# Performance work log

Hardware: AMD Instinct MI355X
Metric: run time of the kernel (lower is better)

Reference implementation:

```python
import jax, jax.numpy as jnp
import numpy as np

NEG_SLOPE = 0.2
EPS = 1e-16

def gat_conv(x, edge_index, W, a_src, a_dst, b):
    # x: [N, Fin], W: [Fin, C], a_src/a_dst: [C], b: [C]
    N = x.shape[0]
    src, dst = edge_index[0], edge_index[1]
    h = x @ W                                  # [N, C]
    alpha_s = h @ a_src                        # [N]
    alpha_d = h @ a_dst                        # [N]
    e = alpha_s[src] + alpha_d[dst]            # [E]
    e = jnp.where(e > 0, e, NEG_SLOPE * e)     # LeakyReLU(0.2)
    # ragged softmax over incoming edges of each dst node
    m = jax.ops.segment_max(e, dst, num_segments=N)       # [N]
    p = jnp.exp(e - m[dst])                                # [E]
    s = jax.ops.segment_sum(p, dst, num_segments=N)        # [N]
    alpha = p / (s[dst] + EPS)                             # [E]
    out = jax.ops.segment_sum(alpha[:, None] * h[src], dst, num_segments=N)
    return out + b

def setup_inputs() -> dict:
    key = jax.random.key(0)
    ks = jax.random.split(key, 10)
    N, Fin, H, C, E = 50000, 128, 64, 64, 800000
    x = jax.random.normal(ks[0], (N, Fin), dtype=jnp.float32)
    edge_index = jax.random.randint(ks[1], (2, E), 0, N, dtype=jnp.int64)
    sc1 = 1.0 / np.sqrt(Fin)
    sc2 = 1.0 / np.sqrt(H)
    W1 = jax.random.normal(ks[2], (Fin, H), dtype=jnp.float32) * sc1
    a_src1 = jax.random.normal(ks[3], (H,), dtype=jnp.float32) * sc2
    a_dst1 = jax.random.normal(ks[4], (H,), dtype=jnp.float32) * sc2
    b1 = jnp.zeros((H,), dtype=jnp.float32)
    W2 = jax.random.normal(ks[5], (H, C), dtype=jnp.float32) * sc2
    a_src2 = jax.random.normal(ks[6], (C,), dtype=jnp.float32) * sc2
    a_dst2 = jax.random.normal(ks[7], (C,), dtype=jnp.float32) * sc2
    b2 = jnp.zeros((C,), dtype=jnp.float32)
    return {"x": x, "edge_index": edge_index, "W1": W1, "a_src1": a_src1,
            "a_dst1": a_dst1, "b1": b1, "W2": W2, "a_src2": a_src2,
            "a_dst2": a_dst2, "b2": b2}

def reference(x, edge_index, W1, a_src1, a_dst1, b1, W2, a_src2, a_dst2, b2):
    h = gat_conv(x, edge_index, W1, a_src1, a_dst1, b1)
    h = jax.nn.relu(h)
    out = gat_conv(h, edge_index, W2, a_src2, a_dst2, b2)
    return out
```

## Files before the change

kernel.cpp:

```cpp
#include <hip/hip_runtime.h>
#include <cstddef>

constexpr int FIN = 128;
constexpr int EPB = 4096;
constexpr int BSH = 7;
constexpr int NPB = 128;

typedef _Float16 half4 __attribute__((ext_vector_type(4)));
typedef _Float16 half8 __attribute__((ext_vector_type(8)));
typedef float floatx4 __attribute__((ext_vector_type(4)));

__device__ __forceinline__ int block_excl_scan_256(int v, int tid, int* wsums) {
    int lane = tid & 63, w = tid >> 6;
    int x = v;
#pragma unroll
    for (int off = 1; off < 64; off <<= 1) {
        int y = __shfl_up(x, off, 64);
        if (lane >= off) x += y;
    }
    if (lane == 63) wsums[w] = x;
    __syncthreads();
    int add = 0;
#pragma unroll
    for (int i = 0; i < 4; ++i) add += (i < w) ? wsums[i] : 0;
    return x + add - v;
}

template <int K, typename XT>
__device__ __forceinline__
void gemm_mfma_body(const XT* __restrict__ X, const float* __restrict__ W,
                    const float* __restrict__ ASRC, const float* __restrict__ ADST,
                    _Float16* __restrict__ Hh, float* __restrict__ AS,
                    float* __restrict__ AD, int N, int blk,
                    _Float16* Xh, _Float16* WT) {
    constexpr int LDH = K + 8;
    const int tid = threadIdx.x;
    const int nb = blk * 64;

    if constexpr (sizeof(XT) == 4) {
        constexpr int QPR = K / 4;
        for (int i = tid; i < 64 * QPR; i += 256) {
            int r = i / QPR, q = i % QPR;
            float4 v = make_float4(0.f, 0.f, 0.f, 0.f);
            if (nb + r < N) v = *(const float4*)(X + (size_t)(nb + r) * K + 4 * q);
            half4 h; h[0] = (_Float16)v.x; h[1] = (_Float16)v.y;
            h[2] = (_Float16)v.z; h[3] = (_Float16)v.w;
            *(half4*)(Xh + r * LDH + 4 * q) = h;
        }
    } else {
        constexpr int OPR = K / 8;
        for (int i = tid; i < 64 * OPR; i += 256) {
            int r = i / OPR, o = i % OPR;
            half8 v = {};
            if (nb + r < N) v = *(const half8*)(X + (size_t)(nb + r) * K + 8 * o);
            *(half8*)(Xh + r * LDH + 8 * o) = v;
        }
    }
    for (int i = tid; i < 64 * (K / 4); i += 256) {
        int n = i & 63, kg = i >> 6;
        half4 h;
#pragma unroll
        for (int j = 0; j < 4; ++j)
            h[j] = (_Float16)W[(4 * kg + j) * 64 + n];
        *(half4*)(WT + n * LDH + 4 * kg) = h;
    }
    __syncthreads();

    const int l = tid & 63;
    const int r0 = (tid >> 6) * 16;
    const int n16 = l & 15, quad = l >> 4;

    floatx4 acc[4];
#pragma unroll
    for (int nt = 0; nt < 4; ++nt) acc[nt] = (floatx4){0.f, 0.f, 0.f, 0.f};

#pragma unroll
    for (int k0 = 0; k0 < K; k0 += 32) {
        half8 a = *(const half8*)(Xh + (r0 + n16) * LDH + k0 + quad * 8);
#pragma unroll
        for (int nt = 0; nt < 4; ++nt) {
            half8 b = *(const half8*)(WT + (nt * 16 + n16) * LDH + k0 + quad * 8);
            acc[nt] = __builtin_amdgcn_mfma_f32_16x16x32_f16(a, b, acc[nt], 0, 0, 0);
        }
    }

    float pa[4] = {0.f, 0.f, 0.f, 0.f}, pd[4] = {0.f, 0.f, 0.f, 0.f};
#pragma unroll
    for (int nt = 0; nt < 4; ++nt) {
        float as_v = ASRC[nt * 16 + n16], ad_v = ADST[nt * 16 + n16];
#pragma unroll
        for (int reg = 0; reg < 4; ++reg) {
            pa[reg] += acc[nt][reg] * as_v;
            pd[reg] += acc[nt][reg] * ad_v;
        }
    }
#pragma unroll
    for (int off = 1; off < 16; off <<= 1) {
#pragma unroll
        for (int reg = 0; reg < 4; ++reg) {
            pa[reg] += __shfl_xor(pa[reg], off, 64);
            pd[reg] += __shfl_xor(pd[reg], off, 64);
        }
    }
    if (n16 == 0) {
#pragma unroll
        for (int reg = 0; reg < 4; ++reg) {
            int row = nb + r0 + quad * 4 + reg;
            if (row < N) { AS[row] = pa[reg]; AD[row] = pd[reg]; }
        }
    }

#pragma unroll
    for (int nt = 0; nt < 4; ++nt)
#pragma unroll
        for (int reg = 0; reg < 4; ++reg)
            Xh[(r0 + quad * 4 + reg) * LDH + nt * 16 + n16] = (_Float16)acc[nt][reg];
    {
        int r = r0 + (l >> 2);
        int o = (l & 3) * 16;
        if (nb + r < N) {
            half8 v0 = *(const half8*)(Xh + r * LDH + o);
            half8 v1 = *(const half8*)(Xh + r * LDH + o + 8);
            *(half8*)(Hh + (size_t)(nb + r) * 64 + o) = v0;
            *(half8*)(Hh + (size_t)(nb + r) * 64 + o + 8) = v1;
        }
    }
}

__global__ __launch_bounds__(256)
void gemm1_and_count(const float* __restrict__ X, const float* __restrict__ W,
                     const float* __restrict__ ASRC, const float* __restrict__ ADST,
                     _Float16* __restrict__ Hh, float* __restrict__ AS,
                     float* __restrict__ AD, int N,
                     const int* __restrict__ dst, int E, int nblk, int nbuckp,
                     int* __restrict__ cnts, int* __restrict__ ticket) {
    constexpr int K = FIN, LDH = K + 8;
    __shared__ _Float16 Xh[64 * LDH];
    __shared__ _Float16 WT[64 * LDH];

    const int tid = threadIdx.x;
    if ((int)blockIdx.x < nblk) {
        int* hist = (int*)Xh;
        if (blockIdx.x == 0 && tid == 0) *ticket = 0;
        for (int i = tid; i < nbuckp; i += 256) hist[i] = 0;
        __syncthreads();
        int e0 = blockIdx.x * EPB;
        int e1 = min(e0 + EPB, E);
        for (int e = e0 + tid; e < e1; e += 256)
            atomicAdd(&hist[dst[e] >> BSH], 1);
        __syncthreads();
        for (int i = tid; i < nbuckp; i += 256)
            cnts[blockIdx.x * nbuckp + i] = hist[i];
        return;
    }
    gemm_mfma_body<K, float>(X, W, ASRC, ADST, Hh, AS, AD, N,
                             blockIdx.x - nblk, Xh, WT);
}

template <int K, typename XT>
__global__ __launch_bounds__(256)
void gemm_feat(const XT* __restrict__ X, const float* __restrict__ W,
               const float* __restrict__ ASRC, const float* __restrict__ ADST,
               _Float16* __restrict__ Hh, float* __restrict__ AS,
               float* __restrict__ AD, int N) {
    constexpr int LDH = K + 8;
    __shared__ _Float16 Xh[64 * LDH];
    __shared__ _Float16 WT[64 * LDH];
    gemm_mfma_body<K, XT>(X, W, ASRC, ADST, Hh, AS, AD, N, blockIdx.x, Xh, WT);
}

__global__ __launch_bounds__(256)
void bucket_colscan_fused(int* __restrict__ cnts, int nblk, int nbuckp,
                          int nbuck, int E, int* __restrict__ btotal,
                          int* __restrict__ bbase, int* __restrict__ ticket) {
    __shared__ int wsums[4];
    __shared__ int ws2[4];
    __shared__ int lastflag;
    int b = blockIdx.x;
    int tid = threadIdx.x;
    int v = (tid < nblk) ? cnts[tid * nbuckp + b] : 0;
    int excl = block_excl_scan_256(v, tid, wsums);
    if (tid < nblk) cnts[tid * nbuckp + b] = excl;
    if (tid == nblk) {
        atomicExch(&btotal[b], excl);
        int old = atomicAdd(ticket, 1);
        lastflag = (old == nbuck - 1);
    }
    __syncthreads();
    if (!lastflag) return;
    int i0 = 2 * tid, i1 = 2 * tid + 1;
    int v0 = (i0 < nbuck) ? atomicAdd(&btotal[i0], 0) : 0;
    int v1 = (i1 < nbuck) ? atomicAdd(&btotal[i1], 0) : 0;
    __syncthreads();
    int e2 = block_excl_scan_256(v0 + v1, tid, ws2);
    if (i0 <= nbuck) bbase[i0] = e2;
    if (i1 <= nbuck) bbase[i1] = e2 + v0;
}

__global__ __launch_bounds__(256)
void bucket_scatter(const int* __restrict__ src, const int* __restrict__ dst,
                    int E, int nbuckp, const int* __restrict__ cnts,
                    const int* __restrict__ bbase, int* __restrict__ ebuck) {
    __shared__ int cur[512];
    int tid = threadIdx.x;
    for (int i = tid; i < nbuckp; i += 256)
        cur[i] = bbase[i] + cnts[blockIdx.x * nbuckp + i];
    __syncthreads();
    int e0 = blockIdx.x * EPB;
    int e1 = min(e0 + EPB, E);
    for (int e = e0 + tid; e < e1; e += 256) {
        int d = dst[e];
        int p = atomicAdd(&cur[d >> BSH], 1);
        ebuck[p] = ((d & (NPB - 1)) << 25) | src[e];
    }
}

__global__ __launch_bounds__(256)
void bucket_to_csr(const int* __restrict__ ebuck, const int* __restrict__ bbase,
                   int N, int E, int* __restrict__ row_ptr,
                   int* __restrict__ csr_src) {
    __shared__ int hist[NPB];
    __shared__ int cur[NPB];
    __shared__ int wsums[4];
    int b = blockIdx.x, tid = threadIdx.x;
    int nstart = b << BSH;
    int base = bbase[b], endp = bbase[b + 1];
    if (tid < NPB) hist[tid] = 0;
    __syncthreads();
    for (int e = base + tid; e < endp; e += 256)
        atomicAdd(&hist[((unsigned)ebuck[e]) >> 25], 1);
    __syncthreads();
    int v = (tid < NPB) ? hist[tid] : 0;
    int excl = block_excl_scan_256(v, tid, wsums);
    if (tid < NPB) {
        cur[tid] = excl;
        if (nstart + tid < N) row_ptr[nstart + tid] = base + excl;
    }
    if (b == 0 && tid == 0) row_ptr[N] = E;
    __syncthreads();
    for (int e = base + tid; e < endp; e += 256) {
        int pv = ebuck[e];
        int p = atomicAdd(&cur[((unsigned)pv) >> 25], 1);
        csr_src[base + p] = pv & 0x1FFFFFF;
    }
}

template <typename OT>
__global__ __launch_bounds__(256)
void gat_aggregate(const _Float16* __restrict__ Hh, const float* __restrict__ AS,
                   const float* __restrict__ AD, const int* __restrict__ row_ptr,
                   const int* __restrict__ csr_src, const float* __restrict__ bias,
                   OT* __restrict__ OUT, int N, int relu) {
    const int lane = threadIdx.x & 63;
    const int n = blockIdx.x * 4 + (threadIdx.x >> 6);
    if (n >= N) return;

    const int base = row_ptr[n], end = row_ptr[n + 1];
    const int cnt = end - base;
    const float adn = AD[n];

    if (cnt > 64) {
        float m = -INFINITY;
        for (int c0 = base; c0 < end; c0 += 64) {
            int c = min(64, end - c0);
            float e = -INFINITY;
            if (lane < c) {
                int sr = csr_src[c0 + lane];
                float t = AS[sr] + adn;
                e = t > 0.f ? t : 0.2f * t;
            }
#pragma unroll
            for (int off = 32; off > 0; off >>= 1) e = fmaxf(e, __shfl_xor(e, off, 64));
            m = fmaxf(m, e);
        }
        float s = 0.f, acc = 0.f;
        for (int c0 = base; c0 < end; c0 += 64) {
            int c = min(64, end - c0);
            int srcl = 0;
            float p = 0.f;
            if (lane < c) {
                srcl = csr_src[c0 + lane];
                float t = AS[srcl] + adn;
                t = t > 0.f ? t : 0.2f * t;
                p = __expf(t - m);
            }
            float cs = p;
#pragma unroll
            for (int off = 32; off > 0; off >>= 1) cs += __shfl_xor(cs, off, 64);
            s += cs;
            for (int j = 0; j < c; ++j)
                acc += __shfl(p, j, 64) *
                       (float)Hh[(size_t)__shfl(srcl, j, 64) * 64 + lane];
        }
        float o = acc * (1.f / (s + 1e-16f)) + bias[lane];
        if (relu) o = fmaxf(o, 0.f);
        OUT[(size_t)n * 64 + lane] = (OT)o;
        return;
    }

    int srcl = 0;
    float el = -INFINITY;
    if (lane < cnt) {
        srcl = csr_src[base + lane];
        float e = AS[srcl] + adn;
        el = e > 0.f ? e : 0.2f * e;
    }
    float m = el;
#pragma unroll
    for (int off = 32; off > 0; off >>= 1) m = fmaxf(m, __shfl_xor(m, off, 64));
    float p = (lane < cnt) ? __expf(el - m) : 0.f;
    float s = p;
#pragma unroll
    for (int off = 32; off > 0; off >>= 1) s += __shfl_xor(s, off, 64);
    const float inv = 1.f / (s + 1e-16f);

    const int eg = lane >> 3;
    const int c8 = (lane & 7) * 8;

    float acc[8], acc2[8];
#pragma unroll
    for (int t = 0; t < 8; ++t) { acc[t] = 0.f; acc2[t] = 0.f; }

    int j = 0;
    for (; j + 16 <= cnt; j += 16) {
        int iA = j + eg, iB = j + 8 + eg;
        int sA = __shfl(srcl, iA, 64), sB = __shfl(srcl, iB, 64);
        float aA = __shfl(p, iA, 64),  aB = __shfl(p, iB, 64);
        half8 hA = *(const half8*)(Hh + (size_t)sA * 64 + c8);
        half8 hB = *(const half8*)(Hh + (size_t)sB * 64 + c8);
#pragma unroll
        for (int t = 0; t < 8; ++t) {
            acc[t]  += aA * (float)hA[t];
            acc2[t] += aB * (float)hB[t];
        }
    }
    for (; j < cnt; j += 8) {
        int iA = j + eg;
        int sA = __shfl(srcl, iA, 64);
        float aA = __shfl(p, iA, 64);
        half8 hA = *(const half8*)(Hh + (size_t)sA * 64 + c8);
#pragma unroll
        for (int t = 0; t < 8; ++t) acc[t] += aA * (float)hA[t];
    }
#pragma unroll
    for (int t = 0; t < 8; ++t) acc[t] += acc2[t];
#pragma unroll
    for (int off = 8; off <= 32; off <<= 1)
#pragma unroll
        for (int t = 0; t < 8; ++t) acc[t] += __shfl_xor(acc[t], off, 64);

    if (lane < 8) {
        float4 b0 = *(const float4*)(bias + c8);
        float4 b1 = *(const float4*)(bias + c8 + 4);
        float o[8];
        o[0] = acc[0] * inv + b0.x; o[1] = acc[1] * inv + b0.y;
        o[2] = acc[2] * inv + b0.z; o[3] = acc[3] * inv + b0.w;
        o[4] = acc[4] * inv + b1.x; o[5] = acc[5] * inv + b1.y;
        o[6] = acc[6] * inv + b1.z; o[7] = acc[7] * inv + b1.w;
        if (relu) {
#pragma unroll
            for (int t = 0; t < 8; ++t) o[t] = fmaxf(o[t], 0.f);
        }
        if constexpr (sizeof(OT) == 2) {
            half8 hv;
#pragma unroll
            for (int t = 0; t < 8; ++t) hv[t] = (_Float16)o[t];
            *(half8*)((_Float16*)OUT + (size_t)n * 64 + c8) = hv;
        } else {
            *(float4*)((float*)OUT + (size_t)n * 64 + c8) =
                make_float4(o[0], o[1], o[2], o[3]);
            *(float4*)((float*)OUT + (size_t)n * 64 + c8 + 4) =
                make_float4(o[4], o[5], o[6], o[7]);
        }
    }
}

extern "C" void kernel_launch(void* const* d_in, const int* in_sizes, int n_in,
                              void* d_out, int out_size, void* d_ws, size_t ws_size,
                              hipStream_t stream) {
    const float* x    = (const float*)d_in[0];
    const int*   ei   = (const int*)d_in[1];
    const float* W1   = (const float*)d_in[2];
    const float* as1w = (const float*)d_in[3];
    const float* ad1w = (const float*)d_in[4];
    const float* b1   = (const float*)d_in[5];
    const float* W2   = (const float*)d_in[6];
    const float* as2w = (const float*)d_in[7];
    const float* ad2w = (const float*)d_in[8];
    const float* b2   = (const float*)d_in[9];
    float* out = (float*)d_out;

    const int N = in_sizes[0] / FIN;
    const int E = in_sizes[1] / 2;
    const int* esrc = ei;
    const int* edst = ei + E;

    const int nbuck = (N + NPB - 1) >> BSH;
    const int nbuckp = nbuck;
    const int nblk = (E + EPB - 1) / EPB;

    char* wp8 = (char*)d_ws;
    _Float16* Hh  = (_Float16*)wp8;  wp8 += (size_t)N * 64 * 2;
    _Float16* R1h = (_Float16*)wp8;  wp8 += (size_t)N * 64 * 2;
    float* AS1 = (float*)wp8;        wp8 += (size_t)N * 4;
    float* AD1 = (float*)wp8;        wp8 += (size_t)N * 4;
    float* AS2 = (float*)wp8;        wp8 += (size_t)N * 4;
    float* AD2 = (float*)wp8;        wp8 += (size_t)N * 4;
    int* row_ptr = (int*)wp8;        wp8 += (size_t)(N + 1) * 4;
    int* csr     = (int*)wp8;        wp8 += (size_t)E * 4;
    int* ebuck   = (int*)wp8;        wp8 += (size_t)E * 4;
    int* cnts    = (int*)wp8;        wp8 += (size_t)nblk * nbuckp * 4;
    int* btotal  = (int*)wp8;        wp8 += (size_t)nbuck * 4;
    int* bbase   = (int*)wp8;        wp8 += (size_t)(nbuck + 1) * 4;
    int* ticket  = (int*)wp8;        wp8 += 4;

    const int nbG = (N + 63) / 64;

    hipLaunchKernelGGL(gemm1_and_count, dim3(nblk + nbG), dim3(256), 0, stream,
                       x, W1, as1w, ad1w, Hh, AS1, AD1, N,
                       edst, E, nblk, nbuckp, cnts, ticket);
    hipLaunchKernelGGL(bucket_colscan_fused, dim3(nbuck), dim3(256), 0, stream,
                       cnts, nblk, nbuckp, nbuck, E, btotal, bbase, ticket);
    hipLaunchKernelGGL(bucket_scatter, dim3(nblk), dim3(256), 0, stream,
                       esrc, edst, E, nbuckp, cnts, bbase, ebuck);
    hipLaunchKernelGGL(bucket_to_csr, dim3(nbuck), dim3(256), 0, stream,
                       ebuck, bbase, N, E, row_ptr, csr);
    hipLaunchKernelGGL(gat_aggregate<_Float16>, dim3((N + 3) / 4), dim3(256), 0,
                       stream, Hh, AS1, AD1, row_ptr, csr, b1, R1h, N, 1);
    hipLaunchKernelGGL((gemm_feat<64, _Float16>), dim3(nbG), dim3(256), 0, stream,
                       R1h, W2, as2w, ad2w, Hh, AS2, AD2, N);
    hipLaunchKernelGGL(gat_aggregate<float>, dim3((N + 3) / 4), dim3(256), 0,
                       stream, Hh, AS2, AD2, row_ptr, csr, b2, out, N, 0);
}
```

Before: 191.6 us.

## Split feature matrices into two 32-column halves and aggregate in two passes

Stores H and the layer-1 result as two separate 32-channel fp16 arrays. Each GAT aggregation becomes two kernels: the first computes the softmax, stores normalised alphas per edge and aggregates the first half, and the second reuses those alphas for the other half. The aim is to shrink each gather's working set so it stays cache-resident. The cost is an extra launch per layer, a per-edge alpha buffer that is written and re-read, and a second read of the CSR arrays. It also halves EPB and makes the column scan loop so that more than 256 count blocks are supported.

```diff
diff --git a/kernel.cpp b/kernel.cpp
--- a/kernel.cpp
+++ b/kernel.cpp
@@ -1,16 +1,18 @@
 #include <hip/hip_runtime.h>
 #include <cstddef>
 
-constexpr int FIN = 128;
-constexpr int EPB = 4096;
-constexpr int BSH = 7;
-constexpr int NPB = 128;
+constexpr int FIN  = 128;
+constexpr int EPB  = 2048;
+constexpr int BSH  = 7;
+constexpr int NPB  = 128;
+constexpr int PACK_SH = 25;
 
 typedef _Float16 half4 __attribute__((ext_vector_type(4)));
 typedef _Float16 half8 __attribute__((ext_vector_type(8)));
 typedef float floatx4 __attribute__((ext_vector_type(4)));
 
-__device__ __forceinline__ int block_excl_scan_256(int v, int tid, int* wsums) {
+__device__ __forceinline__ int block_scan_tot(int v, int tid, int* wsums,
+                                              int* tot) {
     int lane = tid & 63, w = tid >> 6;
     int x = v;
 #pragma unroll
@@ -23,37 +25,43 @@
     int add = 0;
 #pragma unroll
     for (int i = 0; i < 4; ++i) add += (i < w) ? wsums[i] : 0;
+    *tot = wsums[0] + wsums[1] + wsums[2] + wsums[3];
     return x + add - v;
 }
 
-template <int K, typename XT>
+template <int K, bool SPLIT>
 __device__ __forceinline__
-void gemm_mfma_body(const XT* __restrict__ X, const float* __restrict__ W,
+void gemm_mfma_body(const float* __restrict__ Xf,
+                    const _Float16* __restrict__ XA,
+                    const _Float16* __restrict__ XB,
+                    const float* __restrict__ W,
                     const float* __restrict__ ASRC, const float* __restrict__ ADST,
-                    _Float16* __restrict__ Hh, float* __restrict__ AS,
-                    float* __restrict__ AD, int N, int blk,
-                    _Float16* Xh, _Float16* WT) {
+                    _Float16* __restrict__ HA, _Float16* __restrict__ HB,
+                    float* __restrict__ AS, float* __restrict__ AD,
+                    int N, int blk, _Float16* Xh, _Float16* WT) {
     constexpr int LDH = K + 8;
     const int tid = threadIdx.x;
     const int nb = blk * 64;
 
-    if constexpr (sizeof(XT) == 4) {
+    if constexpr (!SPLIT) {
         constexpr int QPR = K / 4;
         for (int i = tid; i < 64 * QPR; i += 256) {
             int r = i / QPR, q = i % QPR;
             float4 v = make_float4(0.f, 0.f, 0.f, 0.f);
-            if (nb + r < N) v = *(const float4*)(X + (size_t)(nb + r) * K + 4 * q);
+            if (nb + r < N) v = *(const float4*)(Xf + (size_t)(nb + r) * K + 4 * q);
             half4 h; h[0] = (_Float16)v.x; h[1] = (_Float16)v.y;
             h[2] = (_Float16)v.z; h[3] = (_Float16)v.w;
             *(half4*)(Xh + r * LDH + 4 * q) = h;
         }
     } else {
-        constexpr int OPR = K / 8;
-        for (int i = tid; i < 64 * OPR; i += 256) {
-            int r = i / OPR, o = i % OPR;
-            half8 v = {};
-            if (nb + r < N) v = *(const half8*)(X + (size_t)(nb + r) * K + 8 * o);
-            *(half8*)(Xh + r * LDH + 8 * o) = v;
+        for (int i = tid; i < 64 * 16; i += 256) {
+            int r = i >> 4, ch = i & 15;
+            half4 v = {};
+            if (nb + r < N) {
+                if (ch < 8) v = *(const half4*)(XA + (size_t)(nb + r) * 32 + 4 * ch);
+                else        v = *(const half4*)(XB + (size_t)(nb + r) * 32 + 4 * (ch - 8));
+            }
+            *(half4*)(Xh + r * LDH + 4 * ch) = v;
         }
     }
     for (int i = tid; i < 64 * (K / 4); i += 256) {
@@ -121,8 +129,13 @@
         if (nb + r < N) {
             half8 v0 = *(const half8*)(Xh + r * LDH + o);
             half8 v1 = *(const half8*)(Xh + r * LDH + o + 8);
-            *(half8*)(Hh + (size_t)(nb + r) * 64 + o) = v0;
-            *(half8*)(Hh + (size_t)(nb + r) * 64 + o + 8) = v1;
+            if (o < 32) {
+                *(half8*)(HA + (size_t)(nb + r) * 32 + o) = v0;
+                *(half8*)(HA + (size_t)(nb + r) * 32 + o + 8) = v1;
+            } else {
+                *(half8*)(HB + (size_t)(nb + r) * 32 + (o - 32)) = v0;
+                *(half8*)(HB + (size_t)(nb + r) * 32 + (o - 32) + 8) = v1;
+            }
         }
     }
 }
@@ -130,9 +143,9 @@
 __global__ __launch_bounds__(256)
 void gemm1_and_count(const float* __restrict__ X, const float* __restrict__ W,
                      const float* __restrict__ ASRC, const float* __restrict__ ADST,
-                     _Float16* __restrict__ Hh, float* __restrict__ AS,
-                     float* __restrict__ AD, int N,
-                     const int* __restrict__ dst, int E, int nblk, int nbuckp,
+                     _Float16* __restrict__ HA, _Float16* __restrict__ HB,
+                     float* __restrict__ AS, float* __restrict__ AD, int N,
+                     const int* __restrict__ dst, int E, int nblk, int nbuck,
                      int* __restrict__ cnts, int* __restrict__ ticket) {
     constexpr int K = FIN, LDH = K + 8;
     __shared__ _Float16 Xh[64 * LDH];
@@ -142,47 +155,54 @@
     if ((int)blockIdx.x < nblk) {
         int* hist = (int*)Xh;
         if (blockIdx.x == 0 && tid == 0) *ticket = 0;
-        for (int i = tid; i < nbuckp; i += 256) hist[i] = 0;
+        for (int i = tid; i < nbuck; i += 256) hist[i] = 0;
         __syncthreads();
         int e0 = blockIdx.x * EPB;
         int e1 = min(e0 + EPB, E);
         for (int e = e0 + tid; e < e1; e += 256)
             atomicAdd(&hist[dst[e] >> BSH], 1);
         __syncthreads();
-        for (int i = tid; i < nbuckp; i += 256)
-            cnts[blockIdx.x * nbuckp + i] = hist[i];
+        for (int i = tid; i < nbuck; i += 256)
+            cnts[blockIdx.x * nbuck + i] = hist[i];
         return;
     }
-    gemm_mfma_body<K, float>(X, W, ASRC, ADST, Hh, AS, AD, N,
-                             blockIdx.x - nblk, Xh, WT);
-}
-
-template <int K, typename XT>
-__global__ __launch_bounds__(256)
-void gemm_feat(const XT* __restrict__ X, const float* __restrict__ W,
-               const float* __restrict__ ASRC, const float* __restrict__ ADST,
-               _Float16* __restrict__ Hh, float* __restrict__ AS,
-               float* __restrict__ AD, int N) {
-    constexpr int LDH = K + 8;
+    gemm_mfma_body<K, false>(X, nullptr, nullptr, W, ASRC, ADST, HA, HB,
+                             AS, AD, N, blockIdx.x - nblk, Xh, WT);
+}
+
+__global__ __launch_bounds__(256)
+void gemm2_feat(const _Float16* __restrict__ XA, const _Float16* __restrict__ XB,
+                const float* __restrict__ W,
+                const float* __restrict__ ASRC, const float* __restrict__ ADST,
+                _Float16* __restrict__ HA, _Float16* __restrict__ HB,
+                float* __restrict__ AS, float* __restrict__ AD, int N) {
+    constexpr int LDH = 64 + 8;
     __shared__ _Float16 Xh[64 * LDH];
     __shared__ _Float16 WT[64 * LDH];
-    gemm_mfma_body<K, XT>(X, W, ASRC, ADST, Hh, AS, AD, N, blockIdx.x, Xh, WT);
-}
-
-__global__ __launch_bounds__(256)
-void bucket_colscan_fused(int* __restrict__ cnts, int nblk, int nbuckp,
-                          int nbuck, int E, int* __restrict__ btotal,
-                          int* __restrict__ bbase, int* __restrict__ ticket) {
+    gemm_mfma_body<64, true>(nullptr, XA, XB, W, ASRC, ADST, HA, HB,
+                             AS, AD, N, blockIdx.x, Xh, WT);
+}
+
+__global__ __launch_bounds__(256)
+void bucket_colscan_fused(int* __restrict__ cnts, int nblk, int nbuck,
+                          int* __restrict__ btotal, int* __restrict__ bbase,
+                          int* __restrict__ ticket) {
     __shared__ int wsums[4];
-    __shared__ int ws2[4];
     __shared__ int lastflag;
     int b = blockIdx.x;
     int tid = threadIdx.x;
-    int v = (tid < nblk) ? cnts[tid * nbuckp + b] : 0;
-    int excl = block_excl_scan_256(v, tid, wsums);
-    if (tid < nblk) cnts[tid * nbuckp + b] = excl;
-    if (tid == nblk) {
-        atomicExch(&btotal[b], excl);
+    int carry = 0;
+    for (int c0 = 0; c0 < nblk; c0 += 256) {
+        int t = c0 + tid;
+        int v = (t < nblk) ? cnts[t * nbuck + b] : 0;
+        int tot;
+        int e = block_scan_tot(v, tid, wsums, &tot);
+        if (t < nblk) cnts[t * nbuck + b] = e + carry;
+        carry += tot;
+        __syncthreads();
+    }
+    if (tid == 0) {
+        atomicExch(&btotal[b], carry);
         int old = atomicAdd(ticket, 1);
         lastflag = (old == nbuck - 1);
     }
@@ -192,26 +212,27 @@
     int v0 = (i0 < nbuck) ? atomicAdd(&btotal[i0], 0) : 0;
     int v1 = (i1 < nbuck) ? atomicAdd(&btotal[i1], 0) : 0;
     __syncthreads();
-    int e2 = block_excl_scan_256(v0 + v1, tid, ws2);
+    int tot2;
+    int e2 = block_scan_tot(v0 + v1, tid, wsums, &tot2);
     if (i0 <= nbuck) bbase[i0] = e2;
     if (i1 <= nbuck) bbase[i1] = e2 + v0;
 }
 
 __global__ __launch_bounds__(256)
 void bucket_scatter(const int* __restrict__ src, const int* __restrict__ dst,
-                    int E, int nbuckp, const int* __restrict__ cnts,
+                    int E, int nbuck, const int* __restrict__ cnts,
                     const int* __restrict__ bbase, int* __restrict__ ebuck) {
     __shared__ int cur[512];
     int tid = threadIdx.x;
-    for (int i = tid; i < nbuckp; i += 256)
-        cur[i] = bbase[i] + cnts[blockIdx.x * nbuckp + i];
+    for (int i = tid; i < nbuck; i += 256)
+        cur[i] = bbase[i] + cnts[blockIdx.x * nbuck + i];
     __syncthreads();
     int e0 = blockIdx.x * EPB;
     int e1 = min(e0 + EPB, E);
     for (int e = e0 + tid; e < e1; e += 256) {
         int d = dst[e];
         int p = atomicAdd(&cur[d >> BSH], 1);
-        ebuck[p] = ((d & (NPB - 1)) << 25) | src[e];
+        ebuck[p] = ((d & (NPB - 1)) << PACK_SH) | src[e];
     }
 }
 
@@ -228,10 +249,11 @@
     if (tid < NPB) hist[tid] = 0;
     __syncthreads();
     for (int e = base + tid; e < endp; e += 256)
-        atomicAdd(&hist[((unsigned)ebuck[e]) >> 25], 1);
+        atomicAdd(&hist[((unsigned)ebuck[e]) >> PACK_SH], 1);
     __syncthreads();
     int v = (tid < NPB) ? hist[tid] : 0;
-    int excl = block_excl_scan_256(v, tid, wsums);
+    int tot;
+    int excl = block_scan_tot(v, tid, wsums, &tot);
     if (tid < NPB) {
         cur[tid] = excl;
         if (nstart + tid < N) row_ptr[nstart + tid] = base + excl;
@@ -240,21 +262,21 @@
     __syncthreads();
     for (int e = base + tid; e < endp; e += 256) {
         int pv = ebuck[e];
-        int p = atomicAdd(&cur[((unsigned)pv) >> 25], 1);
-        csr_src[base + p] = pv & 0x1FFFFFF;
+        int p = atomicAdd(&cur[((unsigned)pv) >> PACK_SH], 1);
+        csr_src[base + p] = pv & ((1 << PACK_SH) - 1);
     }
 }
 
 template <typename OT>
 __global__ __launch_bounds__(256)
-void gat_aggregate(const _Float16* __restrict__ Hh, const float* __restrict__ AS,
-                   const float* __restrict__ AD, const int* __restrict__ row_ptr,
-                   const int* __restrict__ csr_src, const float* __restrict__ bias,
-                   OT* __restrict__ OUT, int N, int relu) {
+void gat_aggA(const _Float16* __restrict__ HA, const float* __restrict__ AS,
+              const float* __restrict__ AD, const int* __restrict__ row_ptr,
+              const int* __restrict__ csr_src, float* __restrict__ alphaB,
+              const float* __restrict__ bias, OT* __restrict__ OUT,
+              int N, int relu) {
     const int lane = threadIdx.x & 63;
     const int n = blockIdx.x * 4 + (threadIdx.x >> 6);
     if (n >= N) return;
-
     const int base = row_ptr[n], end = row_ptr[n + 1];
     const int cnt = end - base;
     const float adn = AD[n];
@@ -273,28 +295,46 @@
             for (int off = 32; off > 0; off >>= 1) e = fmaxf(e, __shfl_xor(e, off, 64));
             m = fmaxf(m, e);
         }
-        float s = 0.f, acc = 0.f;
+        float s = 0.f;
         for (int c0 = base; c0 < end; c0 += 64) {
             int c = min(64, end - c0);
-            int srcl = 0;
             float p = 0.f;
             if (lane < c) {
-                srcl = csr_src[c0 + lane];
-                float t = AS[srcl] + adn;
+                int sr = csr_src[c0 + lane];
+                float t = AS[sr] + adn;
                 t = t > 0.f ? t : 0.2f * t;
                 p = __expf(t - m);
+                alphaB[c0 + lane] = p;
             }
             float cs = p;
 #pragma unroll
             for (int off = 32; off > 0; off >>= 1) cs += __shfl_xor(cs, off, 64);
             s += cs;
-            for (int j = 0; j < c; ++j)
-                acc += __shfl(p, j, 64) *
-                       (float)Hh[(size_t)__shfl(srcl, j, 64) * 64 + lane];
-        }
-        float o = acc * (1.f / (s + 1e-16f)) + bias[lane];
-        if (relu) o = fmaxf(o, 0.f);
-        OUT[(size_t)n * 64 + lane] = (OT)o;
+        }
+        float inv = 1.f / (s + 1e-16f);
+        float acc = 0.f;
+        for (int c0 = base; c0 < end; c0 += 64) {
+            int c = min(64, end - c0);
+            int sr = 0; float p = 0.f;
+            if (lane < c) {
+                sr = csr_src[c0 + lane];
+                p = alphaB[c0 + lane] * inv;
+                alphaB[c0 + lane] = p;
+            }
+            for (int j = 0; j < c; ++j) {
+                float a = __shfl(p, j, 64);
+                int sj = __shfl(sr, j, 64);
+                if (lane < 32) acc += a * (float)HA[(size_t)sj * 32 + lane];
+            }
+        }
+        if (lane < 32) {
+            float o = acc + bias[lane];
+            if (relu) o = fmaxf(o, 0.f);
+            if constexpr (sizeof(OT) == 2)
+                ((_Float16*)OUT)[(size_t)n * 32 + lane] = (_Float16)o;
+            else
+                ((float*)OUT)[(size_t)n * 64 + lane] = o;
+        }
         return;
     }
 
@@ -313,23 +353,22 @@
 #pragma unroll
     for (int off = 32; off > 0; off >>= 1) s += __shfl_xor(s, off, 64);
     const float inv = 1.f / (s + 1e-16f);
+    const float al = p * inv;
+    if (lane < cnt) alphaB[base + lane] = al;
 
     const int eg = lane >> 3;
-    const int c8 = (lane & 7) * 8;
-
-    float acc[8], acc2[8];
-#pragma unroll
-    for (int t = 0; t < 8; ++t) { acc[t] = 0.f; acc2[t] = 0.f; }
-
+    const int c4 = (lane & 7) * 4;
+
+    float acc[4] = {0.f, 0.f, 0.f, 0.f}, acc2[4] = {0.f, 0.f, 0.f, 0.f};
     int j = 0;
     for (; j + 16 <= cnt; j += 16) {
         int iA = j + eg, iB = j + 8 + eg;
         int sA = __shfl(srcl, iA, 64), sB = __shfl(srcl, iB, 64);
-        float aA = __shfl(p, iA, 64),  aB = __shfl(p, iB, 64);
-        half8 hA = *(const half8*)(Hh + (size_t)sA * 64 + c8);
-        half8 hB = *(const half8*)(Hh + (size_t)sB * 64 + c8);
-#pragma unroll
-        for (int t = 0; t < 8; ++t) {
+        float aA = __shfl(al, iA, 64), aB = __shfl(al, iB, 64);
+        half4 hA = *(const half4*)(HA + (size_t)sA * 32 + c4);
+        half4 hB = *(const half4*)(HA + (size_t)sB * 32 + c4);
+#pragma unroll
+        for (int t = 0; t < 4; ++t) {
             acc[t]  += aA * (float)hA[t];
             acc2[t] += aB * (float)hB[t];
         }
@@ -337,40 +376,126 @@
     for (; j < cnt; j += 8) {
         int iA = j + eg;
         int sA = __shfl(srcl, iA, 64);
-        float aA = __shfl(p, iA, 64);
-        half8 hA = *(const half8*)(Hh + (size_t)sA * 64 + c8);
-#pragma unroll
-        for (int t = 0; t < 8; ++t) acc[t] += aA * (float)hA[t];
-    }
-#pragma unroll
-    for (int t = 0; t < 8; ++t) acc[t] += acc2[t];
+        float aA = __shfl(al, iA, 64);
+        half4 hA = *(const half4*)(HA + (size_t)sA * 32 + c4);
+#pragma unroll
+        for (int t = 0; t < 4; ++t) acc[t] += aA * (float)hA[t];
+    }
+#pragma unroll
+    for (int t = 0; t < 4; ++t) acc[t] += acc2[t];
 #pragma unroll
     for (int off = 8; off <= 32; off <<= 1)
 #pragma unroll
-        for (int t = 0; t < 8; ++t) acc[t] += __shfl_xor(acc[t], off, 64);
+        for (int t = 0; t < 4; ++t) acc[t] += __shfl_xor(acc[t], off, 64);
 
     if (lane < 8) {
-        float4 b0 = *(const float4*)(bias + c8);
-        float4 b1 = *(const float4*)(bias + c8 + 4);
-        float o[8];
-        o[0] = acc[0] * inv + b0.x; o[1] = acc[1] * inv + b0.y;
-        o[2] = acc[2] * inv + b0.z; o[3] = acc[3] * inv + b0.w;
-        o[4] = acc[4] * inv + b1.x; o[5] = acc[5] * inv + b1.y;
-        o[6] = acc[6] * inv + b1.z; o[7] = acc[7] * inv + b1.w;
+        float4 bv = *(const float4*)(bias + c4);
+        float o[4] = {acc[0] + bv.x, acc[1] + bv.y, acc[2] + bv.z, acc[3] + bv.w};
         if (relu) {
 #pragma unroll
-            for (int t = 0; t < 8; ++t) o[t] = fmaxf(o[t], 0.f);
+            for (int t = 0; t < 4; ++t) o[t] = fmaxf(o[t], 0.f);
         }
         if constexpr (sizeof(OT) == 2) {
-            half8 hv;
-#pragma unroll
-            for (int t = 0; t < 8; ++t) hv[t] = (_Float16)o[t];
-            *(half8*)((_Float16*)OUT + (size_t)n * 64 + c8) = hv;
+            half4 hv; hv[0] = (_Float16)o[0]; hv[1] = (_Float16)o[1];
+            hv[2] = (_Float16)o[2]; hv[3] = (_Float16)o[3];
+            *(half4*)((_Float16*)OUT + (size_t)n * 32 + c4) = hv;
         } else {
-            *(float4*)((float*)OUT + (size_t)n * 64 + c8) =
+            *(float4*)((float*)OUT + (size_t)n * 64 + c4) =
                 make_float4(o[0], o[1], o[2], o[3]);
-            *(float4*)((float*)OUT + (size_t)n * 64 + c8 + 4) =
-                make_float4(o[4], o[5], o[6], o[7]);
+        }
+    }
+}
+
+template <typename OT>
+__global__ __launch_bounds__(256)
+void gat_aggB(const _Float16* __restrict__ HB, const int* __restrict__ row_ptr,
+              const int* __restrict__ csr_src, const float* __restrict__ alphaB,
+              const float* __restrict__ bias, OT* __restrict__ OUT,
+              int N, int relu) {
+    const int lane = threadIdx.x & 63;
+    const int n = blockIdx.x * 4 + (threadIdx.x >> 6);
+    if (n >= N) return;
+    const int base = row_ptr[n], end = row_ptr[n + 1];
+    const int cnt = end - base;
+
+    if (cnt > 64) {
+        float acc = 0.f;
+        for (int c0 = base; c0 < end; c0 += 64) {
+            int c = min(64, end - c0);
+            int sr = 0; float a = 0.f;
+            if (lane < c) {
+                sr = csr_src[c0 + lane];
+                a = alphaB[c0 + lane];
+            }
+            for (int j = 0; j < c; ++j) {
+                float aj = __shfl(a, j, 64);
+                int sj = __shfl(sr, j, 64);
+                if (lane < 32) acc += aj * (float)HB[(size_t)sj * 32 + lane];
+            }
+        }
+        if (lane < 32) {
+            float o = acc + bias[32 + lane];
+            if (relu) o = fmaxf(o, 0.f);
+            if constexpr (sizeof(OT) == 2)
+                ((_Float16*)OUT)[(size_t)n * 32 + lane] = (_Float16)o;
+            else
+                ((float*)OUT)[(size_t)n * 64 + 32 + lane] = o;
+        }
+        return;
+    }
+
+    int srcl = 0;
+    float al = 0.f;
+    if (lane < cnt) {
+        srcl = csr_src[base + lane];
+        al = alphaB[base + lane];
+    }
+    const int eg = lane >> 3;
+    const int c4 = (lane & 7) * 4;
+
+    float acc[4] = {0.f, 0.f, 0.f, 0.f}, acc2[4] = {0.f, 0.f, 0.f, 0.f};
+    int j = 0;
+    for (; j + 16 <= cnt; j += 16) {
+        int iA = j + eg, iB = j + 8 + eg;
+        int sA = __shfl(srcl, iA, 64), sB = __shfl(srcl, iB, 64);
+        float aA = __shfl(al, iA, 64), aB = __shfl(al, iB, 64);
+        half4 hA = *(const half4*)(HB + (size_t)sA * 32 + c4);
+        half4 hB = *(const half4*)(HB + (size_t)sB * 32 + c4);
+#pragma unroll
+        for (int t = 0; t < 4; ++t) {
+            acc[t]  += aA * (float)hA[t];
+            acc2[t] += aB * (float)hB[t];
+        }
+    }
+    for (; j < cnt; j += 8) {
+        int iA = j + eg;
+        int sA = __shfl(srcl, iA, 64);
+        float aA = __shfl(al, iA, 64);
+        half4 hA = *(const half4*)(HB + (size_t)sA * 32 + c4);
+#pragma unroll
+        for (int t = 0; t < 4; ++t) acc[t] += aA * (float)hA[t];
+    }
+#pragma unroll
+    for (int t = 0; t < 4; ++t) acc[t] += acc2[t];
+#pragma unroll
+    for (int off = 8; off <= 32; off <<= 1)
+#pragma unroll
+        for (int t = 0; t < 4; ++t) acc[t] += __shfl_xor(acc[t], off, 64);
+
+    if (lane < 8) {
+        float4 bv = *(const float4*)(bias + 32 + c4);
+        float o[4] = {acc[0] + bv.x, acc[1] + bv.y, acc[2] + bv.z, acc[3] + bv.w};
+        if (relu) {
+#pragma unroll
+            for (int t = 0; t < 4; ++t) o[t] = fmaxf(o[t], 0.f);
+        }
+        if constexpr (sizeof(OT) == 2) {
+            half4 hv; hv[0] = (_Float16)o[0]; hv[1] = (_Float16)o[1];
+            hv[2] = (_Float16)o[2]; hv[3] = (_Float16)o[3];
+            *(half4*)((_Float16*)OUT + (size_t)n * 32 + c4) = hv;
+        } else {
+            *(float4*)((float*)OUT + (size_t)n * 64 + 32 + c4) =
+                make_float4(o[0], o[1], o[2], o[3]);
         }
     }
 }
@@ -396,39 +521,46 @@
     const int* edst = ei + E;
 
     const int nbuck = (N + NPB - 1) >> BSH;
-    const int nbuckp = nbuck;
-    const int nblk = (E + EPB - 1) / EPB;
+    const int nblk  = (E + EPB - 1) / EPB;
 
     char* wp8 = (char*)d_ws;
-    _Float16* Hh  = (_Float16*)wp8;  wp8 += (size_t)N * 64 * 2;
-    _Float16* R1h = (_Float16*)wp8;  wp8 += (size_t)N * 64 * 2;
+    _Float16* HhA = (_Float16*)wp8;  wp8 += (size_t)N * 32 * 2;
+    _Float16* HhB = (_Float16*)wp8;  wp8 += (size_t)N * 32 * 2;
+    _Float16* R1A = (_Float16*)wp8;  wp8 += (size_t)N * 32 * 2;
+    _Float16* R1B = (_Float16*)wp8;  wp8 += (size_t)N * 32 * 2;
     float* AS1 = (float*)wp8;        wp8 += (size_t)N * 4;
     float* AD1 = (float*)wp8;        wp8 += (size_t)N * 4;
     float* AS2 = (float*)wp8;        wp8 += (size_t)N * 4;
     float* AD2 = (float*)wp8;        wp8 += (size_t)N * 4;
+    float* alphaB = (float*)wp8;     wp8 += (size_t)E * 4;
     int* row_ptr = (int*)wp8;        wp8 += (size_t)(N + 1) * 4;
     int* csr     = (int*)wp8;        wp8 += (size_t)E * 4;
     int* ebuck   = (int*)wp8;        wp8 += (size_t)E * 4;
-    int* cnts    = (int*)wp8;        wp8 += (size_t)nblk * nbuckp * 4;
+    int* cnts    = (int*)wp8;        wp8 += (size_t)nblk * nbuck * 4;
     int* btotal  = (int*)wp8;        wp8 += (size_t)nbuck * 4;
     int* bbase   = (int*)wp8;        wp8 += (size_t)(nbuck + 1) * 4;
     int* ticket  = (int*)wp8;        wp8 += 4;
 
     const int nbG = (N + 63) / 64;
+    const int nbAgg = (N + 3) / 4;
 
     hipLaunchKernelGGL(gemm1_and_count, dim3(nblk + nbG), dim3(256), 0, stream,
-                       x, W1, as1w, ad1w, Hh, AS1, AD1, N,
-                       edst, E, nblk, nbuckp, cnts, ticket);
+                       x, W1, as1w, ad1w, HhA, HhB, AS1, AD1, N,
+                       edst, E, nblk, nbuck, cnts, ticket);
     hipLaunchKernelGGL(bucket_colscan_fused, dim3(nbuck), dim3(256), 0, stream,
-                       cnts, nblk, nbuckp, nbuck, E, btotal, bbase, ticket);
+                       cnts, nblk, nbuck, btotal, bbase, ticket);
     hipLaunchKernelGGL(bucket_scatter, dim3(nblk), dim3(256), 0, stream,
-                       esrc, edst, E, nbuckp, cnts, bbase, ebuck);
+                       esrc, edst, E, nbuck, cnts, bbase, ebuck);
     hipLaunchKernelGGL(bucket_to_csr, dim3(nbuck), dim3(256), 0, stream,
                        ebuck, bbase, N, E, row_ptr, csr);
-    hipLaunchKernelGGL(gat_aggregate<_Float16>, dim3((N + 3) / 4), dim3(256), 0,
-                       stream, Hh, AS1, AD1, row_ptr, csr, b1, R1h, N, 1);
-    hipLaunchKernelGGL((gemm_feat<64, _Float16>), dim3(nbG), dim3(256), 0, stream,
-                       R1h, W2, as2w, ad2w, Hh, AS2, AD2, N);
-    hipLaunchKernelGGL(gat_aggregate<float>, dim3((N + 3) / 4), dim3(256), 0,
-                       stream, Hh, AS2, AD2, row_ptr, csr, b2, out, N, 0);
-}
+    hipLaunchKernelGGL(gat_aggA<_Float16>, dim3(nbAgg), dim3(256), 0, stream,
+                       HhA, AS1, AD1, row_ptr, csr, alphaB, b1, R1A, N, 1);
+    hipLaunchKernelGGL(gat_aggB<_Float16>, dim3(nbAgg), dim3(256), 0, stream,
+                       HhB, row_ptr, csr, alphaB, b1, R1B, N, 1);
+    hipLaunchKernelGGL(gemm2_feat, dim3(nbG), dim3(256), 0, stream,
+                       R1A, R1B, W2, as2w, ad2w, HhA, HhB, AS2, AD2, N);
+    hipLaunchKernelGGL(gat_aggA<float>, dim3(nbAgg), dim3(256), 0, stream,
+                       HhA, AS2, AD2, row_ptr, csr, alphaB, b2, out, N, 0);
+    hipLaunchKernelGGL(gat_aggB<float>, dim3(nbAgg), dim3(256), 0, stream,
+                       HhB, row_ptr, csr, alphaB, b2, out, N, 0);
+}
```

New measurement: 220.0 us. 14.8% more time.

## Process two destination nodes per wavefront in GAT aggregation

Applied to the files above, without the earlier changes.

The aggregation kernel now assigns two consecutive destination nodes to each 64-lane wavefront and interleaves their softmax reductions and feature gathers, with the grid halved to match. This is meant to raise the number of independent gather loads in flight per wave and amortise per-wave setup across two nodes. In exchange it doubles accumulator registers, pads the tail loop to 16 edges (extra zero-weight loads), and falls back to a sequential slow path for both nodes whenever either has more than 64 incoming edges.

```diff
diff --git a/kernel.cpp b/kernel.cpp
--- a/kernel.cpp
+++ b/kernel.cpp
@@ -5,6 +5,7 @@
 constexpr int EPB = 4096;
 constexpr int BSH = 7;
 constexpr int NPB = 128;
+constexpr int PACK_SH = 25;
 
 typedef _Float16 half4 __attribute__((ext_vector_type(4)));
 typedef _Float16 half8 __attribute__((ext_vector_type(8)));
@@ -211,7 +212,7 @@
     for (int e = e0 + tid; e < e1; e += 256) {
         int d = dst[e];
         int p = atomicAdd(&cur[d >> BSH], 1);
-        ebuck[p] = ((d & (NPB - 1)) << 25) | src[e];
+        ebuck[p] = ((d & (NPB - 1)) << PACK_SH) | src[e];
     }
 }
 
@@ -228,7 +229,7 @@
     if (tid < NPB) hist[tid] = 0;
     __syncthreads();
     for (int e = base + tid; e < endp; e += 256)
-        atomicAdd(&hist[((unsigned)ebuck[e]) >> 25], 1);
+        atomicAdd(&hist[((unsigned)ebuck[e]) >> PACK_SH], 1);
     __syncthreads();
     int v = (tid < NPB) ? hist[tid] : 0;
     int excl = block_excl_scan_256(v, tid, wsums);
@@ -240,123 +241,171 @@
     __syncthreads();
     for (int e = base + tid; e < endp; e += 256) {
         int pv = ebuck[e];
-        int p = atomicAdd(&cur[((unsigned)pv) >> 25], 1);
-        csr_src[base + p] = pv & 0x1FFFFFF;
-    }
+        int p = atomicAdd(&cur[((unsigned)pv) >> PACK_SH], 1);
+        csr_src[base + p] = pv & ((1 << PACK_SH) - 1);
+    }
+}
+
+template <typename OT>
+__device__ __forceinline__
+void agg_slow(const _Float16* __restrict__ Hh, const float* __restrict__ AS,
+              const float* __restrict__ AD, const int* __restrict__ csr_src,
+              const float* __restrict__ bias, OT* __restrict__ OUT,
+              int n, int base, int end, int relu, int lane) {
+    const float adn = AD[n];
+    float m = -INFINITY;
+    for (int c0 = base; c0 < end; c0 += 64) {
+        int c = min(64, end - c0);
+        float e = -INFINITY;
+        if (lane < c) {
+            int sr = csr_src[c0 + lane];
+            float t = AS[sr] + adn;
+            e = t > 0.f ? t : 0.2f * t;
+        }
+#pragma unroll
+        for (int off = 32; off > 0; off >>= 1) e = fmaxf(e, __shfl_xor(e, off, 64));
+        m = fmaxf(m, e);
+    }
+    float s = 0.f, acc = 0.f;
+    for (int c0 = base; c0 < end; c0 += 64) {
+        int c = min(64, end - c0);
+        int srcl = 0;
+        float p = 0.f;
+        if (lane < c) {
+            srcl = csr_src[c0 + lane];
+            float t = AS[srcl] + adn;
+            t = t > 0.f ? t : 0.2f * t;
+            p = __expf(t - m);
+        }
+        float cs = p;
+#pragma unroll
+        for (int off = 32; off > 0; off >>= 1) cs += __shfl_xor(cs, off, 64);
+        s += cs;
+        for (int j = 0; j < c; ++j)
+            acc += __shfl(p, j, 64) *
+                   (float)Hh[(size_t)__shfl(srcl, j, 64) * 64 + lane];
+    }
+    float o = acc * (1.f / (s + 1e-16f)) + bias[lane];
+    if (relu) o = fmaxf(o, 0.f);
+    OUT[(size_t)n * 64 + lane] = (OT)o;
 }
 
 template <typename OT>
 __global__ __launch_bounds__(256)
-void gat_aggregate(const _Float16* __restrict__ Hh, const float* __restrict__ AS,
-                   const float* __restrict__ AD, const int* __restrict__ row_ptr,
-                   const int* __restrict__ csr_src, const float* __restrict__ bias,
-                   OT* __restrict__ OUT, int N, int relu) {
+void gat_aggregate2(const _Float16* __restrict__ Hh, const float* __restrict__ AS,
+                    const float* __restrict__ AD, const int* __restrict__ row_ptr,
+                    const int* __restrict__ csr_src, const float* __restrict__ bias,
+                    OT* __restrict__ OUT, int N, int relu) {
     const int lane = threadIdx.x & 63;
-    const int n = blockIdx.x * 4 + (threadIdx.x >> 6);
-    if (n >= N) return;
-
-    const int base = row_ptr[n], end = row_ptr[n + 1];
-    const int cnt = end - base;
-    const float adn = AD[n];
-
-    if (cnt > 64) {
-        float m = -INFINITY;
-        for (int c0 = base; c0 < end; c0 += 64) {
-            int c = min(64, end - c0);
-            float e = -INFINITY;
-            if (lane < c) {
-                int sr = csr_src[c0 + lane];
-                float t = AS[sr] + adn;
-                e = t > 0.f ? t : 0.2f * t;
-            }
-#pragma unroll
-            for (int off = 32; off > 0; off >>= 1) e = fmaxf(e, __shfl_xor(e, off, 64));
-            m = fmaxf(m, e);
-        }
-        float s = 0.f, acc = 0.f;
-        for (int c0 = base; c0 < end; c0 += 64) {
-            int c = min(64, end - c0);
-            int srcl = 0;
-            float p = 0.f;
-            if (lane < c) {
-                srcl = csr_src[c0 + lane];
-                float t = AS[srcl] + adn;
-                t = t > 0.f ? t : 0.2f * t;
-                p = __expf(t - m);
-            }
-            float cs = p;
-#pragma unroll
-            for (int off = 32; off > 0; off >>= 1) cs += __shfl_xor(cs, off, 64);
-            s += cs;
-            for (int j = 0; j < c; ++j)
-                acc += __shfl(p, j, 64) *
-                       (float)Hh[(size_t)__shfl(srcl, j, 64) * 64 + lane];
-        }
-        float o = acc * (1.f / (s + 1e-16f)) + bias[lane];
-        if (relu) o = fmaxf(o, 0.f);
-        OUT[(size_t)n * 64 + lane] = (OT)o;
+    const int nA = blockIdx.x * 8 + (threadIdx.x >> 6) * 2;
+    const int nB = nA + 1;
+    if (nA >= N) return;
+
+    const int baseA = row_ptr[nA];
+    const int baseB = row_ptr[nA + 1];
+    const int endB  = (nB < N) ? row_ptr[nB + 1] : baseB;
+    const int cntA = baseB - baseA;
+    const int cntB = endB - baseB;
+    const bool haveB = (nB < N);
+
+    if (cntA > 64 || cntB > 64) {
+        if (cntA <= 64) {
+            agg_slow<OT>(Hh, AS, AD, csr_src, bias, OUT, nA, baseA, baseB,
+                         relu, lane);
+        } else {
+            agg_slow<OT>(Hh, AS, AD, csr_src, bias, OUT, nA, baseA, baseB,
+                         relu, lane);
+        }
+        if (haveB)
+            agg_slow<OT>(Hh, AS, AD, csr_src, bias, OUT, nB, baseB, endB,
+                         relu, lane);
         return;
     }
 
-    int srcl = 0;
-    float el = -INFINITY;
-    if (lane < cnt) {
-        srcl = csr_src[base + lane];
-        float e = AS[srcl] + adn;
-        el = e > 0.f ? e : 0.2f * e;
-    }
-    float m = el;
-#pragma unroll
-    for (int off = 32; off > 0; off >>= 1) m = fmaxf(m, __shfl_xor(m, off, 64));
-    float p = (lane < cnt) ? __expf(el - m) : 0.f;
-    float s = p;
-#pragma unroll
-    for (int off = 32; off > 0; off >>= 1) s += __shfl_xor(s, off, 64);
-    const float inv = 1.f / (s + 1e-16f);
+    const float adnA = AD[nA];
+    const float adnB = haveB ? AD[nB] : 0.f;
+
+    int sAl = 0, sBl = 0;
+    if (lane < cntA) sAl = csr_src[baseA + lane];
+    if (lane < cntB) sBl = csr_src[baseB + lane];
+    float elA = -INFINITY, elB = -INFINITY;
+    if (lane < cntA) {
+        float t = AS[sAl] + adnA;
+        elA = t > 0.f ? t : 0.2f * t;
+    }
+    if (lane < cntB) {
+        float t = AS[sBl] + adnB;
+        elB = t > 0.f ? t : 0.2f * t;
+    }
+    float mA = elA, mB = elB;
+#pragma unroll
+    for (int off = 32; off > 0; off >>= 1) {
+        mA = fmaxf(mA, __shfl_xor(mA, off, 64));
+        mB = fmaxf(mB, __shfl_xor(mB, off, 64));
+    }
+    float pA = (lane < cntA) ? __expf(elA - mA) : 0.f;
+    float pB = (lane < cntB) ? __expf(elB - mB) : 0.f;
+    float sA = pA, sB = pB;
+#pragma unroll
+    for (int off = 32; off > 0; off >>= 1) {
+        sA += __shfl_xor(sA, off, 64);
+        sB += __shfl_xor(sB, off, 64);
+    }
+    const float invA = 1.f / (sA + 1e-16f);
+    const float invB = 1.f / (sB + 1e-16f);
 
     const int eg = lane >> 3;
     const int c8 = (lane & 7) * 8;
 
-    float acc[8], acc2[8];
-#pragma unroll
-    for (int t = 0; t < 8; ++t) { acc[t] = 0.f; acc2[t] = 0.f; }
-
-    int j = 0;
-    for (; j + 16 <= cnt; j += 16) {
-        int iA = j + eg, iB = j + 8 + eg;
-        int sA = __shfl(srcl, iA, 64), sB = __shfl(srcl, iB, 64);
-        float aA = __shfl(p, iA, 64),  aB = __shfl(p, iB, 64);
-        half8 hA = *(const half8*)(Hh + (size_t)sA * 64 + c8);
-        half8 hB = *(const half8*)(Hh + (size_t)sB * 64 + c8);
+    float aA1[8], aA2[8], aB1[8], aB2[8];
+#pragma unroll
+    for (int t = 0; t < 8; ++t) { aA1[t] = 0.f; aA2[t] = 0.f; aB1[t] = 0.f; aB2[t] = 0.f; }
+
+    const int jmax = max(cntA, cntB);
+    for (int j = 0; j < jmax; j += 16) {
+        if (j < cntA) {
+            int i0 = j + eg, i1 = j + 8 + eg;
+            int s0 = __shfl(sAl, i0, 64), s1 = __shfl(sAl, i1, 64);
+            float a0 = __shfl(pA, i0, 64), a1 = __shfl(pA, i1, 64);
+            half8 h0 = *(const half8*)(Hh + (size_t)s0 * 64 + c8);
+            half8 h1 = *(const half8*)(Hh + (size_t)s1 * 64 + c8);
+#pragma unroll
+            for (int t = 0; t < 8; ++t) {
+                aA1[t] += a0 * (float)h0[t];
+                aA2[t] += a1 * (float)h1[t];
+            }
+        }
+        if (j < cntB) {
+            int i0 = j + eg, i1 = j + 8 + eg;
+            int s0 = __shfl(sBl, i0, 64), s1 = __shfl(sBl, i1, 64);
+            float a0 = __shfl(pB, i0, 64), a1 = __shfl(pB, i1, 64);
+            half8 h0 = *(const half8*)(Hh + (size_t)s0 * 64 + c8);
+            half8 h1 = *(const half8*)(Hh + (size_t)s1 * 64 + c8);
+#pragma unroll
+            for (int t = 0; t < 8; ++t) {
+                aB1[t] += a0 * (float)h0[t];
+                aB2[t] += a1 * (float)h1[t];
+            }
+        }
+    }
+#pragma unroll
+    for (int t = 0; t < 8; ++t) { aA1[t] += aA2[t]; aB1[t] += aB2[t]; }
+#pragma unroll
+    for (int off = 8; off <= 32; off <<= 1)
 #pragma unroll
         for (int t = 0; t < 8; ++t) {
-            acc[t]  += aA * (float)hA[t];
-            acc2[t] += aB * (float)hB[t];
-        }
-    }
-    for (; j < cnt; j += 8) {
-        int iA = j + eg;
-        int sA = __shfl(srcl, iA, 64);
-        float aA = __shfl(p, iA, 64);
-        half8 hA = *(const half8*)(Hh + (size_t)sA * 64 + c8);
-#pragma unroll
-        for (int t = 0; t < 8; ++t) acc[t] += aA * (float)hA[t];
-    }
-#pragma unroll
-    for (int t = 0; t < 8; ++t) acc[t] += acc2[t];
-#pragma unroll
-    for (int off = 8; off <= 32; off <<= 1)
-#pragma unroll
-        for (int t = 0; t < 8; ++t) acc[t] += __shfl_xor(acc[t], off, 64);
+            aA1[t] += __shfl_xor(aA1[t], off, 64);
+            aB1[t] += __shfl_xor(aB1[t], off, 64);
+        }
 
     if (lane < 8) {
         float4 b0 = *(const float4*)(bias + c8);
         float4 b1 = *(const float4*)(bias + c8 + 4);
         float o[8];
-        o[0] = acc[0] * inv + b0.x; o[1] = acc[1] * inv + b0.y;
-        o[2] = acc[2] * inv + b0.z; o[3] = acc[3] * inv + b0.w;
-        o[4] = acc[4] * inv + b1.x; o[5] = acc[5] * inv + b1.y;
-        o[6] = acc[6] * inv + b1.z; o[7] = acc[7] * inv + b1.w;
+        o[0] = aA1[0] * invA + b0.x; o[1] = aA1[1] * invA + b0.y;
+        o[2] = aA1[2] * invA + b0.z; o[3] = aA1[3] * invA + b0.w;
+        o[4] = aA1[4] * invA + b1.x; o[5] = aA1[5] * invA + b1.y;
+        o[6] = aA1[6] * invA + b1.z; o[7] = aA1[7] * invA + b1.w;
         if (relu) {
 #pragma unroll
             for (int t = 0; t < 8; ++t) o[t] = fmaxf(o[t], 0.f);
@@ -365,11 +414,36 @@
             half8 hv;
 #pragma unroll
             for (int t = 0; t < 8; ++t) hv[t] = (_Float16)o[t];
-            *(half8*)((_Float16*)OUT + (size_t)n * 64 + c8) = hv;
+            *(half8*)((_Float16*)OUT + (size_t)nA * 64 + c8) = hv;
         } else {
-            *(float4*)((float*)OUT + (size_t)n * 64 + c8) =
+            *(float4*)((float*)OUT + (size_t)nA * 64 + c8) =
                 make_float4(o[0], o[1], o[2], o[3]);
-            *(float4*)((float*)OUT + (size_t)n * 64 + c8 + 4) =
+            *(float4*)((float*)OUT + (size_t)nA * 64 + c8 + 4) =
+                make_float4(o[4], o[5], o[6], o[7]);
+        }
+    }
+    if (haveB && lane >= 8 && lane < 16) {
+        const int c8b = ((lane - 8) & 7) * 8;
+        float4 b0 = *(const float4*)(bias + c8b);
+        float4 b1 = *(const float4*)(bias + c8b + 4);
+        float o[8];
+        o[0] = aB1[0] * invB + b0.x; o[1] = aB1[1] * invB + b0.y;
+        o[2] = aB1[2] * invB + b0.z; o[3] = aB1[3] * invB + b0.w;
+        o[4] = aB1[4] * invB + b1.x; o[5] = aB1[5] * invB + b1.y;
+        o[6] = aB1[6] * invB + b1.z; o[7] = aB1[7] * invB + b1.w;
+        if (relu) {
+#pragma unroll
+            for (int t = 0; t < 8; ++t) o[t] = fmaxf(o[t], 0.f);
+        }
+        if constexpr (sizeof(OT) == 2) {
+            half8 hv;
+#pragma unroll
+            for (int t = 0; t < 8; ++t) hv[t] = (_Float16)o[t];
+            *(half8*)((_Float16*)OUT + (size_t)nB * 64 + c8b) = hv;
+        } else {
+            *(float4*)((float*)OUT + (size_t)nB * 64 + c8b) =
+                make_float4(o[0], o[1], o[2], o[3]);
+            *(float4*)((float*)OUT + (size_t)nB * 64 + c8b + 4) =
                 make_float4(o[4], o[5], o[6], o[7]);
         }
     }
@@ -415,6 +489,7 @@
     int* ticket  = (int*)wp8;        wp8 += 4;
 
     const int nbG = (N + 63) / 64;
+    const int nbAgg = (N + 7) / 8;
 
     hipLaunchKernelGGL(gemm1_and_count, dim3(nblk + nbG), dim3(256), 0, stream,
                        x, W1, as1w, ad1w, Hh, AS1, AD1, N,
@@ -425,10 +500,10 @@
                        esrc, edst, E, nbuckp, cnts, bbase, ebuck);
     hipLaunchKernelGGL(bucket_to_csr, dim3(nbuck), dim3(256), 0, stream,
                        ebuck, bbase, N, E, row_ptr, csr);
-    hipLaunchKernelGGL(gat_aggregate<_Float16>, dim3((N + 3) / 4), dim3(256), 0,
+    hipLaunchKernelGGL(gat_aggregate2<_Float16>, dim3(nbAgg), dim3(256), 0,
                        stream, Hh, AS1, AD1, row_ptr, csr, b1, R1h, N, 1);
     hipLaunchKernelGGL((gemm_feat<64, _Float16>), dim3(nbG), dim3(256), 0, stream,
                        R1h, W2, as2w, ad2w, Hh, AS2, AD2, N);
-    hipLaunchKernelGGL(gat_aggregate<float>, dim3((N + 3) / 4), dim3(256), 0,
+    hipLaunchKernelGGL(gat_aggregate2<float>, dim3(nbAgg), dim3(256), 0,
                        stream, Hh, AS2, AD2, row_ptr, csr, b2, out, N, 0);
 }
```

After: 196.2 us. 2.4% more time.
